# Performance work log

Hardware: AMD Instinct MI355X
Metric: run time of the kernel (lower is better)

Reference implementation:

```python
import jax, jax.numpy as jnp
import numpy as np

B, T, C, H = 8, 2048, 1024, 64
SCALE = H ** -0.5


def setup_inputs() -> dict:
    key = jax.random.key(0)
    kx, kq, kk, kv = jax.random.split(key, 4)
    x = jax.random.normal(kx, (B, T, C), dtype=jnp.float32)
    w_q = jax.random.normal(kq, (C, H), dtype=jnp.float32) * (C ** -0.5)
    w_k = jax.random.normal(kk, (C, H), dtype=jnp.float32) * (C ** -0.5)
    w_v = jax.random.normal(kv, (C, H), dtype=jnp.float32) * (C ** -0.5)
    return {"x": x, "w_q": w_q, "w_k": w_k, "w_v": w_v}


def reference(x, w_q, w_k, w_v):
    # Projections: [B,T,C] @ [C,H] -> [B,T,H]
    q = jnp.einsum('btc,ch->bth', x, w_q)
    k = jnp.einsum('btc,ch->bth', x, w_k)
    v = jnp.einsum('btc,ch->bth', x, w_v)
    # Scaled scores [B,T,T], causal mask, softmax (dropout p=0 -> identity)
    wei = jnp.einsum('bqh,bkh->bqk', q, k) * SCALE
    tq = x.shape[1]
    causal = jnp.tril(jnp.ones((tq, tq), dtype=bool))
    wei = jnp.where(causal[None, :, :], wei, -jnp.inf)
    wei = jax.nn.softmax(wei, axis=-1)
    out = jnp.einsum('bqk,bkh->bqh', wei, v)
    return out
```

## Files before the change

### kernel.cpp

```cpp
#include <hip/hip_runtime.h>
#include <hip/hip_bf16.h>
#include <cstdint>

#define TB 8
#define TT 2048
#define TC 1024
#define TH 64

typedef __bf16 bf16;
typedef __bf16 bf16x2 __attribute__((ext_vector_type(2)));
typedef __bf16 bf16x4 __attribute__((ext_vector_type(4)));
typedef __bf16 bf16x8 __attribute__((ext_vector_type(8)));
typedef float  f32x4  __attribute__((ext_vector_type(4)));

constexpr float QSCALE = 0.125f * 1.44269504088896340736f;

__device__ __forceinline__ void gll16(const void* g, void* l) {
    __builtin_amdgcn_global_load_lds((const __attribute__((address_space(1))) unsigned int*)g,
                                     (__attribute__((address_space(3))) unsigned int*)l, 16, 0, 0);
}

#define WAIT_VM0()   __builtin_amdgcn_s_waitcnt(0x0F70)
#define WAIT_VM8()   __builtin_amdgcn_s_waitcnt(0x0F78)
#define WAIT_LGKM0() __builtin_amdgcn_s_waitcnt(0xC07F)

__global__ void prep_wT(const float* __restrict__ wq, const float* __restrict__ wk,
                        const float* __restrict__ wv, bf16* __restrict__ wT) {
    int idx = blockIdx.x * blockDim.x + threadIdx.x;
    if (idx >= 3 * TH * TC) return;
    int wsel = idx / (TH * TC);
    int rem  = idx % (TH * TC);
    int c = rem / TH;
    int h = rem % TH;
    const float* w = (wsel == 0) ? wq : (wsel == 1) ? wk : wv;
    wT[(size_t)wsel * TH * TC + (size_t)h * TC + c] = (bf16)w[(size_t)c * TH + h];
}

__launch_bounds__(512)
__global__ void proj(const float* __restrict__ x, const bf16* __restrict__ wT,
                     bf16* __restrict__ Q, bf16* __restrict__ K, bf16* __restrict__ VT) {
    __shared__ __align__(16) char lds[81920];
    const int tid  = threadIdx.x;
    const int wv8  = tid >> 6;
    const int lane = tid & 63;
    const int quad = lane >> 4, l16 = lane & 15;
    const int rg   = wv8 & 3;
    const int ch   = wv8 >> 2;
    const int m0   = blockIdx.x * 64;

    const float* xb = x + (size_t)m0 * TC;

    f32x4 acc[6];
#pragma unroll
    for (int g = 0; g < 6; g++) acc[g] = f32x4{0.f, 0.f, 0.f, 0.f};

    const int lr16 = lane >> 4, lc16 = lane & 15;
    const int lr8  = lane >> 3, lc8  = lane & 7;

#define STAGE(kc, bb)                                                          \
    {                                                                          \
        _Pragma("unroll")                                                      \
        for (int i = 0; i < 2; i++) {            \
            int base_row = wv8 * 8 + i * 4;                                    \
            int row = base_row + lr16;                                         \
            int c = lc16 ^ (row & 15);                                         \
            gll16(xb + (size_t)row * TC + (kc) * 64 + c * 4,                   \
                  lds + (bb) * 16384 + base_row * 256);                        \
        }                                                                      \
        _Pragma("unroll")                                                      \
        for (int j = 0; j < 3; j++) {            \
            int idx = wv8 * 3 + j;                                             \
            int w = idx >> 3;                                                  \
            int base_col = (idx & 7) * 8;                                      \
            int col = base_col + lr8;                                          \
            int c = lc8 ^ (col & 7);                                           \
            gll16(wT + (size_t)w * TH * TC + (size_t)col * TC + (kc) * 64 + c * 8, \
                  lds + 32768 + (bb) * 24576 + (w * 64 + base_col) * 128);     \
        }                                                                      \
    }

    STAGE(0, 0);
    for (int kc = 0; kc < 16; kc++) {
        const int cur = kc & 1;
        __syncthreads();
        if (kc + 1 < 16) STAGE(kc + 1, cur ^ 1);
        const char* Xb = lds + cur * 16384;
        const char* Wb = lds + 32768 + cur * 24576;
        const int row = rg * 16 + l16;
#pragma unroll
        for (int s = 0; s < 2; s++) {
            int c1 = (s * 8 + 2 * quad) ^ l16;
            int c2 = (s * 8 + 2 * quad + 1) ^ l16;
            f32x4 a0 = *(const f32x4*)(Xb + row * 256 + c1 * 16);
            f32x4 a1 = *(const f32x4*)(Xb + row * 256 + c2 * 16);
            bf16x8 af;
            af[0] = (bf16)a0[0]; af[1] = (bf16)a0[1]; af[2] = (bf16)a0[2]; af[3] = (bf16)a0[3];
            af[4] = (bf16)a1[0]; af[5] = (bf16)a1[1]; af[6] = (bf16)a1[2]; af[7] = (bf16)a1[3];
#pragma unroll
            for (int g = 0; g < 6; g++) {
                int cg = ch * 6 + g;
                int w = cg >> 2;
                int col = (cg & 3) * 16 + l16;
                int c = (s * 4 + quad) ^ (col & 7);
                bf16x8 bq = *(const bf16x8*)(Wb + (w * 64 + col) * 128 + c * 16);
                acc[g] = __builtin_amdgcn_mfma_f32_16x16x32_bf16(af, bq, acc[g], 0, 0, 0);
            }
        }
    }

    const int mrow = m0 + rg * 16 + quad * 4;
    const int b = m0 >> 11;
    const int t = mrow & 2047;
#pragma unroll
    for (int g = 0; g < 6; g++) {
        int cg = ch * 6 + g;
        int w = cg >> 2;
        int col = (cg & 3) * 16 + l16;
        if (w == 0) {
#pragma unroll
            for (int r = 0; r < 4; r++)
                Q[(size_t)(mrow + r) * TH + col] = (bf16)(acc[g][r] * QSCALE);
        } else if (w == 1) {
#pragma unroll
            for (int r = 0; r < 4; r++)
                K[(size_t)(mrow + r) * TH + col] = (bf16)acc[g][r];
        } else {
            bf16x4 o;
#pragma unroll
            for (int r = 0; r < 4; r++) o[r] = (bf16)acc[g][r];
            *(bf16x4*)(VT + ((size_t)b * TH + col) * TT + t) = o;
        }
    }
}
#undef STAGE

__device__ __forceinline__ float packbf(float a, float b) {
    union { bf16x2 h; float f; } u;
    u.h[0] = (bf16)a; u.h[1] = (bf16)b;
    return u.f;
}

__launch_bounds__(256, 2)
__global__ void attn(const bf16* __restrict__ Q, const bf16* __restrict__ K,
                     const bf16* __restrict__ VT, float* __restrict__ out) {
    __shared__ __align__(16) char lds[65536];

    const int tid  = threadIdx.x;
    const int wv   = tid >> 6;
    const int lane = tid & 63;
    const int quad = lane >> 4, l16 = lane & 15;
    const int b  = blockIdx.x & 7;
    const int qc = 63 - (blockIdx.x >> 3);
    const int q0 = qc * 32;

    char* Kst = lds + wv * 16384;
    char* Vst = Kst + 8192;

    const bf16* Qb = Q  + (size_t)b * TT * TH;
    const bf16* Kb = K  + (size_t)b * TT * TH;
    const bf16* Vb = VT + (size_t)b * TH * TT;

    bf16x8 bq[2][2];
#pragma unroll
    for (int qg = 0; qg < 2; qg++)
#pragma unroll
        for (int kh = 0; kh < 2; kh++)
            bq[qg][kh] = *(const bf16x8*)(Qb + (size_t)(q0 + qg * 16 + l16) * TH + kh * 32 + quad * 8);

    f32x4 accO[2][4];
#pragma unroll
    for (int qg = 0; qg < 2; qg++)
#pragma unroll
        for (int g = 0; g < 4; g++) accO[qg][g] = f32x4{0.f, 0.f, 0.f, 0.f};
    float lIp[2] = {0.f, 0.f};

    const int r8 = lane >> 3, c8 = lane & 7;
    const int r4 = lane >> 2, c4 = lane & 3;
    const int src1 = (quad & 1) * 32 + l16;
    const int src2 = src1 + 16;

#define STAGEKV(kt_, bb_)                                                       \
    {                                                                           \
        const int k0_ = (kt_) * 32;                                             \
        _Pragma("unroll")                                                       \
        for (int i = 0; i < 4; i++) {                                           \
            int t = i * 8 + r8;                                                 \
            gll16(Kb + (size_t)(k0_ + t) * 64 + ((c8 ^ r8) * 8),                \
                  Kst + (bb_) * 4096 + i * 1024);                               \
        }                                                                       \
        _Pragma("unroll")                                                       \
        for (int i = 0; i < 4; i++) {                                           \
            int h = i * 16 + r4;                                                \
            gll16(Vb + (size_t)h * TT + k0_ + ((c4 ^ quad) * 8),                \
                  Vst + (bb_) * 4096 + i * 1024);                               \
        }                                                                       \
    }

    if (wv <= qc) {
        const int kt1 = (wv + 4 <= qc) ? wv + 4 : qc;
        STAGEKV(wv, 0);
        STAGEKV(kt1, 1);
        int nit = 0;
        for (int kt = wv; kt <= qc; kt += 4, nit++) {
            const int bb = nit & 1;
            WAIT_VM8();

            bf16x8 ka[2][2], bv[4];
#pragma unroll
            for (int g = 0; g < 2; g++) {
                int t = g * 16 + l16;
                const char* kr = Kst + bb * 4096 + t * 128;
                ka[g][0] = *(const bf16x8*)(kr + (((quad) ^ (t & 7)) << 4));
                ka[g][1] = *(const bf16x8*)(kr + (((4 + quad) ^ (t & 7)) << 4));
            }
#pragma unroll
            for (int g = 0; g < 4; g++) {
                int h = g * 16 + l16;
                bv[g] = *(const bf16x8*)(Vst + bb * 4096 + h * 64 + ((quad ^ (l16 >> 2)) << 4));
            }
            WAIT_LGKM0();
            {
                int ktn = kt + 8; if (ktn > qc) ktn = qc;
                STAGEKV(ktn, bb);
            }

            f32x4 s[2][2];
#pragma unroll
            for (int g = 0; g < 2; g++)
#pragma unroll
                for (int qg = 0; qg < 2; qg++) {
                    f32x4 t0 = f32x4{0.f, 0.f, 0.f, 0.f};
                    t0 = __builtin_amdgcn_mfma_f32_16x16x32_bf16(ka[g][0], bq[qg][0], t0, 0, 0, 0);
                    t0 = __builtin_amdgcn_mfma_f32_16x16x32_bf16(ka[g][1], bq[qg][1], t0, 0, 0, 0);
                    s[qg][g] = t0;
                }

            if (kt == qc) {
#pragma unroll
                for (int qg = 0; qg < 2; qg++) {
                    const int ql = qg * 16 + l16;
#pragma unroll
                    for (int g = 0; g < 2; g++)
#pragma unroll
                        for (int r = 0; r < 4; r++)
                            if (g * 16 + quad * 4 + r > ql) s[qg][g][r] = -3.0e38f;
                }
            }

#pragma unroll
            for (int qg = 0; qg < 2; qg++) {
                float rs = 0.f;
#pragma unroll
                for (int g = 0; g < 2; g++)
#pragma unroll
                    for (int r = 0; r < 4; r++) {
                        float p = __builtin_amdgcn_exp2f(s[qg][g][r]);
                        s[qg][g][r] = p;
                        rs += p;
                    }
                lIp[qg] += rs;
            }

#pragma unroll
            for (int qg = 0; qg < 2; qg++) {
                float p00 = packbf(s[qg][0][0], s[qg][0][1]);
                float p01 = packbf(s[qg][0][2], s[qg][0][3]);
                float p10 = packbf(s[qg][1][0], s[qg][1][1]);
                float p11 = packbf(s[qg][1][2], s[qg][1][3]);
                float A0p0 = __shfl(p00, src1), A0p1 = __shfl(p01, src1);
                float B0p0 = __shfl(p00, src2), B0p1 = __shfl(p01, src2);
                float A1p0 = __shfl(p10, src1), A1p1 = __shfl(p11, src1);
                float B1p0 = __shfl(p10, src2), B1p1 = __shfl(p11, src2);
                bool lo = quad < 2;
                union { float4 f; bf16x8 v; } u;
                u.f = make_float4(lo ? A0p0 : A1p0, lo ? A0p1 : A1p1,
                                  lo ? B0p0 : B1p0, lo ? B0p1 : B1p1);
#pragma unroll
                for (int g = 0; g < 4; g++)
                    accO[qg][g] = __builtin_amdgcn_mfma_f32_16x16x32_bf16(u.v, bv[g], accO[qg][g], 0, 0, 0);
            }
        }
    }
#undef STAGEKV

    float lI[2];
#pragma unroll
    for (int qg = 0; qg < 2; qg++) {
        float l = lIp[qg];
        l += __shfl_xor(l, 16);
        l += __shfl_xor(l, 32);
        lI[qg] = l;
    }

    WAIT_VM0();
    __syncthreads();
    float* Omg = (float*)lds;
    float* Lmg = (float*)(lds + 34816);
#pragma unroll
    for (int qg = 0; qg < 2; qg++)
#pragma unroll
        for (int g = 0; g < 4; g++)
#pragma unroll
            for (int r = 0; r < 4; r++)
                Omg[(size_t)(wv * 32 + qg * 16 + quad * 4 + r) * 68 + g * 16 + l16] = accO[qg][g][r];
    if (quad == 0) {
#pragma unroll
        for (int qg = 0; qg < 2; qg++)
            Lmg[wv * 32 + qg * 16 + l16] = lI[qg];
    }
    __syncthreads();

#pragma unroll
    for (int p = 0; p < 2; p++) {
        const int idx = p * 256 + tid;
        const int q = idx >> 4;
        const int hs = (idx & 15) * 4;
        float denom = 0.f, o0 = 0.f, o1 = 0.f, o2 = 0.f, o3 = 0.f;
#pragma unroll
        for (int w = 0; w < 4; w++) {
            denom += Lmg[w * 32 + q];
            const float* op = Omg + (size_t)(w * 32 + q) * 68 + hs;
            o0 += op[0]; o1 += op[1]; o2 += op[2]; o3 += op[3];
        }
        float inv = 1.f / denom;
        *(float4*)(out + ((size_t)b * TT + q0 + q) * TH + hs) =
            make_float4(o0 * inv, o1 * inv, o2 * inv, o3 * inv);
    }
}

extern "C" void kernel_launch(void* const* d_in, const int* in_sizes, int n_in,
                              void* d_out, int out_size, void* d_ws, size_t ws_size,
                              hipStream_t stream) {
    const float* x  = (const float*)d_in[0];
    const float* wq = (const float*)d_in[1];
    const float* wk = (const float*)d_in[2];
    const float* wv = (const float*)d_in[3];

    char* ws = (char*)d_ws;
    bf16*  wT = (bf16*)(ws);
    bf16*  Q  = (bf16*)(ws + 393216);
    bf16*  K  = (bf16*)(ws + 2490368);
    bf16*  VT = (bf16*)(ws + 4587520);
    float* out = (float*)d_out;

    hipLaunchKernelGGL(prep_wT, dim3(768), dim3(256), 0, stream, wq, wk, wv, wT);
    hipLaunchKernelGGL(proj, dim3(256), dim3(512), 0, stream, x, wT, Q, K, VT);
    hipLaunchKernelGGL(attn, dim3(TB * 64), dim3(256), 0, stream, Q, K, VT, out);
}
```

Before: 127.4 us.

## Pair complementary causal query tiles in one 512-thread attention block

```diff
diff --git a/kernel.cpp b/kernel.cpp
--- a/kernel.cpp
+++ b/kernel.cpp
@@ -140,17 +140,20 @@
     return u.f;
 }
 
-__launch_bounds__(256, 2)
+__launch_bounds__(512, 2)
 __global__ void attn(const bf16* __restrict__ Q, const bf16* __restrict__ K,
                      const bf16* __restrict__ VT, float* __restrict__ out) {
-    __shared__ __align__(16) char lds[65536];
+    __shared__ __align__(16) char lds[131072];
 
     const int tid  = threadIdx.x;
     const int wv   = tid >> 6;
+    const int wvl  = wv & 3;
+    const int grp  = wv >> 2;
     const int lane = tid & 63;
     const int quad = lane >> 4, l16 = lane & 15;
     const int b  = blockIdx.x & 7;
-    const int qc = 63 - (blockIdx.x >> 3);
+    const int j  = blockIdx.x >> 3;
+    const int qc = grp ? (63 - j) : j;
     const int q0 = qc * 32;
 
     char* Kst = lds + wv * 16384;
@@ -196,12 +199,12 @@
         }                                                                       \
     }
 
-    if (wv <= qc) {
-        const int kt1 = (wv + 4 <= qc) ? wv + 4 : qc;
-        STAGEKV(wv, 0);
+    if (wvl <= qc) {
+        const int kt1 = (wvl + 4 <= qc) ? wvl + 4 : qc;
+        STAGEKV(wvl, 0);
         STAGEKV(kt1, 1);
         int nit = 0;
-        for (int kt = wv; kt <= qc; kt += 4, nit++) {
+        for (int kt = wvl; kt <= qc; kt += 4, nit++) {
             const int bb = nit & 1;
             WAIT_VM8();
 
@@ -294,36 +297,41 @@
 
     WAIT_VM0();
     __syncthreads();
-    float* Omg = (float*)lds;
-    float* Lmg = (float*)(lds + 34816);
+    float* Omg = (float*)(lds + grp * 34816);
+    float* Lmg = (float*)(lds + 69632 + grp * 512);
 #pragma unroll
     for (int qg = 0; qg < 2; qg++)
 #pragma unroll
         for (int g = 0; g < 4; g++)
 #pragma unroll
             for (int r = 0; r < 4; r++)
-                Omg[(size_t)(wv * 32 + qg * 16 + quad * 4 + r) * 68 + g * 16 + l16] = accO[qg][g][r];
+                Omg[(size_t)(wvl * 32 + qg * 16 + quad * 4 + r) * 68 + g * 16 + l16] = accO[qg][g][r];
     if (quad == 0) {
 #pragma unroll
         for (int qg = 0; qg < 2; qg++)
-            Lmg[wv * 32 + qg * 16 + l16] = lI[qg];
+            Lmg[wvl * 32 + qg * 16 + l16] = lI[qg];
     }
     __syncthreads();
 
 #pragma unroll
     for (int p = 0; p < 2; p++) {
-        const int idx = p * 256 + tid;
-        const int q = idx >> 4;
-        const int hs = (idx & 15) * 4;
+        const int idx = p * 512 + tid;
+        const int c  = idx >> 9;
+        const int wi = idx & 511;
+        const int q  = wi >> 4;
+        const int hs = (wi & 15) * 4;
+        const float* Om = (const float*)(lds + c * 34816);
+        const float* Lm = (const float*)(lds + 69632 + c * 512);
         float denom = 0.f, o0 = 0.f, o1 = 0.f, o2 = 0.f, o3 = 0.f;
 #pragma unroll
         for (int w = 0; w < 4; w++) {
-            denom += Lmg[w * 32 + q];
-            const float* op = Omg + (size_t)(w * 32 + q) * 68 + hs;
+            denom += Lm[w * 32 + q];
+            const float* op = Om + (size_t)(w * 32 + q) * 68 + hs;
             o0 += op[0]; o1 += op[1]; o2 += op[2]; o3 += op[3];
         }
         float inv = 1.f / denom;
-        *(float4*)(out + ((size_t)b * TT + q0 + q) * TH + hs) =
+        const int q0c = (c ? (63 - j) : j) * 32;
+        *(float4*)(out + ((size_t)b * TT + q0c + q) * TH + hs) =
             make_float4(o0 * inv, o1 * inv, o2 * inv, o3 * inv);
     }
 }
@@ -345,5 +353,5 @@
 
     hipLaunchKernelGGL(prep_wT, dim3(768), dim3(256), 0, stream, wq, wk, wv, wT);
     hipLaunchKernelGGL(proj, dim3(256), dim3(512), 0, stream, x, wT, Q, K, VT);
-    hipLaunchKernelGGL(attn, dim3(TB * 64), dim3(256), 0, stream, Q, K, VT, out);
-}
+    hipLaunchKernelGGL(attn, dim3(TB * 32), dim3(512), 0, stream, Q, K, VT, out);
+}
```

New measurement: 126.7 us. About the same (-0.6%).

## Replace LDS-staged K/V pipeline with direct register double-buffered global loads

Applied to the files above, without the earlier changes.

```diff
diff --git a/kernel.cpp b/kernel.cpp
--- a/kernel.cpp
+++ b/kernel.cpp
@@ -19,10 +19,6 @@
     __builtin_amdgcn_global_load_lds((const __attribute__((address_space(1))) unsigned int*)g,
                                      (__attribute__((address_space(3))) unsigned int*)l, 16, 0, 0);
 }
-
-#define WAIT_VM0()   __builtin_amdgcn_s_waitcnt(0x0F70)
-#define WAIT_VM8()   __builtin_amdgcn_s_waitcnt(0x0F78)
-#define WAIT_LGKM0() __builtin_amdgcn_s_waitcnt(0xC07F)
 
 __global__ void prep_wT(const float* __restrict__ wq, const float* __restrict__ wk,
                         const float* __restrict__ wv, bf16* __restrict__ wT) {
@@ -140,10 +136,10 @@
     return u.f;
 }
 
-__launch_bounds__(256, 2)
+__launch_bounds__(256, 3)
 __global__ void attn(const bf16* __restrict__ Q, const bf16* __restrict__ K,
                      const bf16* __restrict__ VT, float* __restrict__ out) {
-    __shared__ __align__(16) char lds[65536];
+    __shared__ __align__(16) char lds[35328];
 
     const int tid  = threadIdx.x;
     const int wv   = tid >> 6;
@@ -153,9 +149,6 @@
     const int qc = 63 - (blockIdx.x >> 3);
     const int q0 = qc * 32;
 
-    char* Kst = lds + wv * 16384;
-    char* Vst = Kst + 8192;
-
     const bf16* Qb = Q  + (size_t)b * TT * TH;
     const bf16* Kb = K  + (size_t)b * TT * TH;
     const bf16* Vb = VT + (size_t)b * TH * TT;
@@ -174,114 +167,101 @@
         for (int g = 0; g < 4; g++) accO[qg][g] = f32x4{0.f, 0.f, 0.f, 0.f};
     float lIp[2] = {0.f, 0.f};
 
-    const int r8 = lane >> 3, c8 = lane & 7;
-    const int r4 = lane >> 2, c4 = lane & 3;
     const int src1 = (quad & 1) * 32 + l16;
     const int src2 = src1 + 16;
 
-#define STAGEKV(kt_, bb_)                                                       \
+#define LOADT(KA, BV, kt_)                                                      \
     {                                                                           \
         const int k0_ = (kt_) * 32;                                             \
         _Pragma("unroll")                                                       \
-        for (int i = 0; i < 4; i++) {                                           \
-            int t = i * 8 + r8;                                                 \
-            gll16(Kb + (size_t)(k0_ + t) * 64 + ((c8 ^ r8) * 8),                \
-                  Kst + (bb_) * 4096 + i * 1024);                               \
+        for (int g = 0; g < 2; g++) {                                           \
+            const bf16* kr = Kb + (size_t)(k0_ + g * 16 + l16) * 64 + quad * 8; \
+            KA[g][0] = *(const bf16x8*)(kr);                                    \
+            KA[g][1] = *(const bf16x8*)(kr + 32);                               \
         }                                                                       \
         _Pragma("unroll")                                                       \
-        for (int i = 0; i < 4; i++) {                                           \
-            int h = i * 16 + r4;                                                \
-            gll16(Vb + (size_t)h * TT + k0_ + ((c4 ^ quad) * 8),                \
-                  Vst + (bb_) * 4096 + i * 1024);                               \
+        for (int g = 0; g < 4; g++)                                             \
+            BV[g] = *(const bf16x8*)(Vb + (size_t)(g * 16 + l16) * TT + k0_ + quad * 8); \
+    }
+
+#define COMPUTE(KA, BV, kt_)                                                    \
+    {                                                                           \
+        f32x4 s[2][2];                                                          \
+        _Pragma("unroll")                                                       \
+        for (int g = 0; g < 2; g++)                                             \
+            _Pragma("unroll")                                                   \
+            for (int qg = 0; qg < 2; qg++) {                                    \
+                f32x4 t0 = f32x4{0.f, 0.f, 0.f, 0.f};                           \
+                t0 = __builtin_amdgcn_mfma_f32_16x16x32_bf16(KA[g][0], bq[qg][0], t0, 0, 0, 0); \
+                t0 = __builtin_amdgcn_mfma_f32_16x16x32_bf16(KA[g][1], bq[qg][1], t0, 0, 0, 0); \
+                s[qg][g] = t0;                                                  \
+            }                                                                   \
+        if ((kt_) == qc) {                                                      \
+            _Pragma("unroll")                                                   \
+            for (int qg = 0; qg < 2; qg++) {                                    \
+                const int ql = qg * 16 + l16;                                   \
+                _Pragma("unroll")                                               \
+                for (int g = 0; g < 2; g++)                                     \
+                    _Pragma("unroll")                                           \
+                    for (int r = 0; r < 4; r++)                                 \
+                        if (g * 16 + quad * 4 + r > ql) s[qg][g][r] = -3.0e38f; \
+            }                                                                   \
         }                                                                       \
+        _Pragma("unroll")                                                       \
+        for (int qg = 0; qg < 2; qg++) {                                        \
+            float rs = 0.f;                                                     \
+            _Pragma("unroll")                                                   \
+            for (int g = 0; g < 2; g++)                                         \
+                _Pragma("unroll")                                               \
+                for (int r = 0; r < 4; r++) {                                   \
+                    float p = __builtin_amdgcn_exp2f(s[qg][g][r]);              \
+                    s[qg][g][r] = p;                                            \
+                    rs += p;                                                    \
+                }                                                               \
+            lIp[qg] += rs;                                                      \
+        }                                                                       \
+        _Pragma("unroll")                                                       \
+        for (int qg = 0; qg < 2; qg++) {                                        \
+            float p00 = packbf(s[qg][0][0], s[qg][0][1]);                       \
+            float p01 = packbf(s[qg][0][2], s[qg][0][3]);                       \
+            float p10 = packbf(s[qg][1][0], s[qg][1][1]);                       \
+            float p11 = packbf(s[qg][1][2], s[qg][1][3]);                       \
+            float A0p0 = __shfl(p00, src1), A0p1 = __shfl(p01, src1);           \
+            float B0p0 = __shfl(p00, src2), B0p1 = __shfl(p01, src2);           \
+            float A1p0 = __shfl(p10, src1), A1p1 = __shfl(p11, src1);           \
+            float B1p0 = __shfl(p10, src2), B1p1 = __shfl(p11, src2);           \
+            bool lo = quad < 2;                                                 \
+            union { float4 f; bf16x8 v; } u;                                    \
+            u.f = make_float4(lo ? A0p0 : A1p0, lo ? A0p1 : A1p1,               \
+                              lo ? B0p0 : B1p0, lo ? B0p1 : B1p1);              \
+            _Pragma("unroll")                                                   \
+            for (int g = 0; g < 4; g++)                                         \
+                accO[qg][g] = __builtin_amdgcn_mfma_f32_16x16x32_bf16(u.v, BV[g], accO[qg][g], 0, 0, 0); \
+        }                                                                       \
     }
 
     if (wv <= qc) {
-        const int kt1 = (wv + 4 <= qc) ? wv + 4 : qc;
-        STAGEKV(wv, 0);
-        STAGEKV(kt1, 1);
-        int nit = 0;
-        for (int kt = wv; kt <= qc; kt += 4, nit++) {
-            const int bb = nit & 1;
-            WAIT_VM8();
-
-            bf16x8 ka[2][2], bv[4];
-#pragma unroll
-            for (int g = 0; g < 2; g++) {
-                int t = g * 16 + l16;
-                const char* kr = Kst + bb * 4096 + t * 128;
-                ka[g][0] = *(const bf16x8*)(kr + (((quad) ^ (t & 7)) << 4));
-                ka[g][1] = *(const bf16x8*)(kr + (((4 + quad) ^ (t & 7)) << 4));
+        bf16x8 kaA[2][2], bvA[4], kaB[2][2], bvB[4];
+        LOADT(kaA, bvA, wv);
+        for (int kt = wv;;) {
+            {
+                int ktn = (kt + 4 <= qc) ? kt + 4 : qc;
+                LOADT(kaB, bvB, ktn);
             }
-#pragma unroll
-            for (int g = 0; g < 4; g++) {
-                int h = g * 16 + l16;
-                bv[g] = *(const bf16x8*)(Vst + bb * 4096 + h * 64 + ((quad ^ (l16 >> 2)) << 4));
+            COMPUTE(kaA, bvA, kt);
+            kt += 4;
+            if (kt > qc) break;
+            {
+                int ktn = (kt + 4 <= qc) ? kt + 4 : qc;
+                LOADT(kaA, bvA, ktn);
             }
-            WAIT_LGKM0();
-            {
-                int ktn = kt + 8; if (ktn > qc) ktn = qc;
-                STAGEKV(ktn, bb);
-            }
-
-            f32x4 s[2][2];
-#pragma unroll
-            for (int g = 0; g < 2; g++)
-#pragma unroll
-                for (int qg = 0; qg < 2; qg++) {
-                    f32x4 t0 = f32x4{0.f, 0.f, 0.f, 0.f};
-                    t0 = __builtin_amdgcn_mfma_f32_16x16x32_bf16(ka[g][0], bq[qg][0], t0, 0, 0, 0);
-                    t0 = __builtin_amdgcn_mfma_f32_16x16x32_bf16(ka[g][1], bq[qg][1], t0, 0, 0, 0);
-                    s[qg][g] = t0;
-                }
-
-            if (kt == qc) {
-#pragma unroll
-                for (int qg = 0; qg < 2; qg++) {
-                    const int ql = qg * 16 + l16;
-#pragma unroll
-                    for (int g = 0; g < 2; g++)
-#pragma unroll
-                        for (int r = 0; r < 4; r++)
-                            if (g * 16 + quad * 4 + r > ql) s[qg][g][r] = -3.0e38f;
-                }
-            }
-
-#pragma unroll
-            for (int qg = 0; qg < 2; qg++) {
-                float rs = 0.f;
-#pragma unroll
-                for (int g = 0; g < 2; g++)
-#pragma unroll
-                    for (int r = 0; r < 4; r++) {
-                        float p = __builtin_amdgcn_exp2f(s[qg][g][r]);
-                        s[qg][g][r] = p;
-                        rs += p;
-                    }
-                lIp[qg] += rs;
-            }
-
-#pragma unroll
-            for (int qg = 0; qg < 2; qg++) {
-                float p00 = packbf(s[qg][0][0], s[qg][0][1]);
-                float p01 = packbf(s[qg][0][2], s[qg][0][3]);
-                float p10 = packbf(s[qg][1][0], s[qg][1][1]);
-                float p11 = packbf(s[qg][1][2], s[qg][1][3]);
-                float A0p0 = __shfl(p00, src1), A0p1 = __shfl(p01, src1);
-                float B0p0 = __shfl(p00, src2), B0p1 = __shfl(p01, src2);
-                float A1p0 = __shfl(p10, src1), A1p1 = __shfl(p11, src1);
-                float B1p0 = __shfl(p10, src2), B1p1 = __shfl(p11, src2);
-                bool lo = quad < 2;
-                union { float4 f; bf16x8 v; } u;
-                u.f = make_float4(lo ? A0p0 : A1p0, lo ? A0p1 : A1p1,
-                                  lo ? B0p0 : B1p0, lo ? B0p1 : B1p1);
-#pragma unroll
-                for (int g = 0; g < 4; g++)
-                    accO[qg][g] = __builtin_amdgcn_mfma_f32_16x16x32_bf16(u.v, bv[g], accO[qg][g], 0, 0, 0);
-            }
+            COMPUTE(kaB, bvB, kt);
+            kt += 4;
+            if (kt > qc) break;
         }
     }
-#undef STAGEKV
+#undef LOADT
+#undef COMPUTE
 
     float lI[2];
 #pragma unroll
@@ -292,8 +272,6 @@
         lI[qg] = l;
     }
 
-    WAIT_VM0();
-    __syncthreads();
     float* Omg = (float*)lds;
     float* Lmg = (float*)(lds + 34816);
 #pragma unroll
```

Measured after the change: 135.1 us. 1.06x slower.

## Triple-buffer projection loads and single-buffer attention KV to raise occupancy

Applied to the files above, without the earlier changes.

```diff
diff --git a/kernel.cpp b/kernel.cpp
--- a/kernel.cpp
+++ b/kernel.cpp
@@ -21,7 +21,7 @@
 }
 
 #define WAIT_VM0()   __builtin_amdgcn_s_waitcnt(0x0F70)
-#define WAIT_VM8()   __builtin_amdgcn_s_waitcnt(0x0F78)
+#define WAIT_VM5()   __builtin_amdgcn_s_waitcnt(0x0F75)
 #define WAIT_LGKM0() __builtin_amdgcn_s_waitcnt(0xC07F)
 
 __global__ void prep_wT(const float* __restrict__ wq, const float* __restrict__ wk,
@@ -39,7 +39,7 @@
 __launch_bounds__(512)
 __global__ void proj(const float* __restrict__ x, const bf16* __restrict__ wT,
                      bf16* __restrict__ Q, bf16* __restrict__ K, bf16* __restrict__ VT) {
-    __shared__ __align__(16) char lds[81920];
+    __shared__ __align__(16) char lds[122880];
     const int tid  = threadIdx.x;
     const int wv8  = tid >> 6;
     const int lane = tid & 63;
@@ -65,7 +65,7 @@
             int row = base_row + lr16;                                         \
             int c = lc16 ^ (row & 15);                                         \
             gll16(xb + (size_t)row * TC + (kc) * 64 + c * 4,                   \
-                  lds + (bb) * 16384 + base_row * 256);                        \
+                  lds + (bb) * 40960 + base_row * 256);                        \
         }                                                                      \
         _Pragma("unroll")                                                      \
         for (int j = 0; j < 3; j++) {            \
@@ -75,17 +75,20 @@
             int col = base_col + lr8;                                          \
             int c = lc8 ^ (col & 7);                                           \
             gll16(wT + (size_t)w * TH * TC + (size_t)col * TC + (kc) * 64 + c * 8, \
-                  lds + 32768 + (bb) * 24576 + (w * 64 + base_col) * 128);     \
+                  lds + (bb) * 40960 + 16384 + (w * 64 + base_col) * 128);     \
         }                                                                      \
     }
 
     STAGE(0, 0);
+    STAGE(1, 1);
     for (int kc = 0; kc < 16; kc++) {
-        const int cur = kc & 1;
-        __syncthreads();
-        if (kc + 1 < 16) STAGE(kc + 1, cur ^ 1);
-        const char* Xb = lds + cur * 16384;
-        const char* Wb = lds + 32768 + cur * 24576;
+        const int cur = kc % 3;
+        if (kc < 15) WAIT_VM5(); else WAIT_VM0();
+        __builtin_amdgcn_s_barrier();
+        __builtin_amdgcn_sched_barrier(0);
+        if (kc + 2 < 16) STAGE(kc + 2, (kc + 2) % 3);
+        const char* Xb = lds + cur * 40960;
+        const char* Wb = lds + cur * 40960 + 16384;
         const int row = rg * 16 + l16;
 #pragma unroll
         for (int s = 0; s < 2; s++) {
@@ -140,10 +143,10 @@
     return u.f;
 }
 
-__launch_bounds__(256, 2)
+__launch_bounds__(256, 3)
 __global__ void attn(const bf16* __restrict__ Q, const bf16* __restrict__ K,
                      const bf16* __restrict__ VT, float* __restrict__ out) {
-    __shared__ __align__(16) char lds[65536];
+    __shared__ __align__(16) char lds[35840];
 
     const int tid  = threadIdx.x;
     const int wv   = tid >> 6;
@@ -153,8 +156,8 @@
     const int qc = 63 - (blockIdx.x >> 3);
     const int q0 = qc * 32;
 
-    char* Kst = lds + wv * 16384;
-    char* Vst = Kst + 8192;
+    char* Kst = lds + wv * 8192;
+    char* Vst = Kst + 4096;
 
     const bf16* Qb = Q  + (size_t)b * TT * TH;
     const bf16* Kb = K  + (size_t)b * TT * TH;
@@ -179,50 +182,43 @@
     const int src1 = (quad & 1) * 32 + l16;
     const int src2 = src1 + 16;
 
-#define STAGEKV(kt_, bb_)                                                       \
+#define STAGEKV(kt_)                                                            \
     {                                                                           \
         const int k0_ = (kt_) * 32;                                             \
         _Pragma("unroll")                                                       \
         for (int i = 0; i < 4; i++) {                                           \
             int t = i * 8 + r8;                                                 \
             gll16(Kb + (size_t)(k0_ + t) * 64 + ((c8 ^ r8) * 8),                \
-                  Kst + (bb_) * 4096 + i * 1024);                               \
+                  Kst + i * 1024);                                              \
         }                                                                       \
         _Pragma("unroll")                                                       \
         for (int i = 0; i < 4; i++) {                                           \
             int h = i * 16 + r4;                                                \
             gll16(Vb + (size_t)h * TT + k0_ + ((c4 ^ quad) * 8),                \
-                  Vst + (bb_) * 4096 + i * 1024);                               \
+                  Vst + i * 1024);                                              \
         }                                                                       \
     }
 
     if (wv <= qc) {
-        const int kt1 = (wv + 4 <= qc) ? wv + 4 : qc;
-        STAGEKV(wv, 0);
-        STAGEKV(kt1, 1);
-        int nit = 0;
-        for (int kt = wv; kt <= qc; kt += 4, nit++) {
-            const int bb = nit & 1;
-            WAIT_VM8();
+        STAGEKV(wv);
+        for (int kt = wv; kt <= qc; kt += 4) {
+            WAIT_VM0();
 
             bf16x8 ka[2][2], bv[4];
 #pragma unroll
             for (int g = 0; g < 2; g++) {
                 int t = g * 16 + l16;
-                const char* kr = Kst + bb * 4096 + t * 128;
+                const char* kr = Kst + t * 128;
                 ka[g][0] = *(const bf16x8*)(kr + (((quad) ^ (t & 7)) << 4));
                 ka[g][1] = *(const bf16x8*)(kr + (((4 + quad) ^ (t & 7)) << 4));
             }
 #pragma unroll
             for (int g = 0; g < 4; g++) {
                 int h = g * 16 + l16;
-                bv[g] = *(const bf16x8*)(Vst + bb * 4096 + h * 64 + ((quad ^ (l16 >> 2)) << 4));
+                bv[g] = *(const bf16x8*)(Vst + h * 64 + ((quad ^ (l16 >> 2)) << 4));
             }
             WAIT_LGKM0();
-            {
-                int ktn = kt + 8; if (ktn > qc) ktn = qc;
-                STAGEKV(ktn, bb);
-            }
+            if (kt + 4 <= qc) STAGEKV(kt + 4);
 
             f32x4 s[2][2];
 #pragma unroll
```

After: 125.5 us. About the same (-1.5%).
